# Optimization experiments

Measured on AMD Instinct MI355X. Metric: run time of the kernel, lower is better.

The kernel has to match this reference:

```python
import jax, jax.numpy as jnp
from jax import lax
import numpy as np

D_MODEL = 1024
EXP = 2
D_INNER = EXP * D_MODEL
D_STATE = 16
D_CONV = 4
DT_RANK = 64  # ceil(d_model/16), mamba default
NUM_GROUPS = 4
BSZ, SEQ = 2, 2048
EPS = 1e-5


def setup_inputs() -> dict:
    key = jax.random.key(0)
    ks = jax.random.split(key, 10)
    def n(k, shape, s=0.02):
        return jax.random.normal(k, shape, jnp.float32) * s
    return dict(
        x=jax.random.normal(ks[0], (BSZ, SEQ, D_MODEL), jnp.float32),
        ln1_g=jnp.ones((D_MODEL,), jnp.float32), ln1_b=jnp.zeros((D_MODEL,), jnp.float32),
        ln2_g=jnp.ones((D_MODEL,), jnp.float32), ln2_b=jnp.zeros((D_MODEL,), jnp.float32),
        W1=n(ks[1], (EXP * D_MODEL, D_MODEL)), b1=jnp.zeros((EXP * D_MODEL,), jnp.float32),
        W2=n(ks[2], (D_MODEL, EXP * D_MODEL)), b2=jnp.zeros((D_MODEL,), jnp.float32),
        in_proj_w=n(ks[3], (2 * D_INNER, D_MODEL)),
        conv_w=n(ks[4], (D_INNER, 1, D_CONV), 0.2), conv_b=jnp.zeros((D_INNER,), jnp.float32),
        x_proj_w=n(ks[5], (DT_RANK + 2 * D_STATE, D_INNER)),
        dt_proj_w=n(ks[6], (D_INNER, DT_RANK), 0.1), dt_proj_b=n(ks[7], (D_INNER,), 0.5),
        A_log=jnp.tile(jnp.log(jnp.arange(1, D_STATE + 1, dtype=jnp.float32)), (D_INNER, 1)),
        D_param=jnp.ones((D_INNER,), jnp.float32),
        out_proj_w=n(ks[8], (D_MODEL, D_INNER)),
    )


def _layernorm(x, g, b):
    m = jnp.mean(x, -1, keepdims=True)
    v = jnp.var(x, -1, keepdims=True)
    return (x - m) * lax.rsqrt(v + EPS) * g + b


def _ste_sign(w):
    # sign quantization with straight-through estimator (groupwise split is a no-op for sign)
    return w + lax.stop_gradient(jnp.sign(w) - w)


def _quant_act_groupwise(x, b=8):
    # groups along seq dim (x.shape[1]); gamma is the abs-max over the whole group slab
    Qb = float(2 ** (b - 1))
    B_, L, D = x.shape
    g = x.reshape(B_, NUM_GROUPS, L // NUM_GROUPS, D)
    gamma = jnp.max(jnp.abs(g), axis=(0, 2, 3), keepdims=True)
    q = jnp.clip(g * Qb / (gamma + EPS), -Qb + EPS, Qb - EPS)
    return q.reshape(B_, L, D)


def _mamba(u, in_proj_w, conv_w, conv_b, x_proj_w, dt_proj_w, dt_proj_b, A_log, D_param, out_proj_w):
    B_, L, _ = u.shape
    xz = u @ in_proj_w.T                         # [B, L, 2*d_inner]
    xs, z = jnp.split(xz, 2, axis=-1)
    # depthwise causal conv1d
    xt = jnp.transpose(xs, (0, 2, 1))            # [B, d_inner, L]
    xt = lax.conv_general_dilated(xt, conv_w, (1,), [(D_CONV - 1, 0)],
                                  feature_group_count=D_INNER,
                                  dimension_numbers=('NCH', 'OIH', 'NCH'))
    xt = xt + conv_b[None, :, None]
    xs = jax.nn.silu(jnp.transpose(xt, (0, 2, 1)))  # [B, L, d_inner]
    x_dbl = xs @ x_proj_w.T                      # [B, L, dt_rank + 2*d_state]
    dt, Bm, Cm = jnp.split(x_dbl, [DT_RANK, DT_RANK + D_STATE], axis=-1)
    dt = jax.nn.softplus(dt @ dt_proj_w.T + dt_proj_b)   # [B, L, d_inner]
    A = -jnp.exp(A_log)                          # [d_inner, d_state]

    def step(h, inp):
        dt_s, B_s, C_s, x_s = inp                # [B,di], [B,ds], [B,ds], [B,di]
        dA = jnp.exp(dt_s[..., None] * A)        # [B, di, ds]
        h = h * dA + (dt_s * x_s)[..., None] * B_s[:, None, :]
        y = jnp.einsum('bds,bs->bd', h, C_s)
        return h, y

    tm = lambda a: jnp.transpose(a, (1, 0, 2))   # time-major
    h0 = jnp.zeros((B_, D_INNER, D_STATE), u.dtype)
    _, ys = lax.scan(step, h0, (tm(dt), tm(Bm), tm(Cm), tm(xs)))
    y = jnp.transpose(ys, (1, 0, 2)) + D_param * xs
    y = y * jax.nn.silu(z)
    return y @ out_proj_w.T


def reference(x, ln1_g, ln1_b, ln2_g, ln2_b, W1, b1, W2, b2,
              in_proj_w, conv_w, conv_b, x_proj_w, dt_proj_w, dt_proj_b,
              A_log, D_param, out_proj_w):
    qW1 = _ste_sign(W1)
    qW2 = _ste_sign(W2)
    gated = jnp.clip(_layernorm(x, ln1_g, ln1_b) @ qW1.T + b1, -1.0, 1.0)  # Hardtanh
    x = x + gated @ qW2.T + b2
    qx = _quant_act_groupwise(x)
    out = qx + _mamba(_layernorm(qx, ln2_g, ln2_b), in_proj_w, conv_w, conv_b,
                      x_proj_w, dt_proj_w, dt_proj_b, A_log, D_param, out_proj_w)
    return out
```

## Files before the change

### kernel.cpp

```cpp
#include <hip/hip_runtime.h>
#include <math.h>

#define D_MODEL 1024
#define D_INNER 2048
#define D_STATE 16
#define DT_RANK 64
#define BSZ 2
#define SEQ 2048
#define NTOK (BSZ*SEQ)
#define NCH  (BSZ*D_INNER)
#define NCHUNK 64
#define CLEN 32
#define EPS 1e-5f

typedef __attribute__((ext_vector_type(8))) short short8v;
typedef __attribute__((ext_vector_type(4))) float f32x4;

__device__ __forceinline__ float sgnf(float w) {
    return (w > 0.f) ? 1.f : ((w < 0.f) ? -1.f : 0.f);
}
__device__ __forceinline__ unsigned short f2bf(float f) {
    unsigned int x = __float_as_uint(f);
    x += 0x7fffu + ((x >> 16) & 1u);
    return (unsigned short)(x >> 16);
}
__device__ __forceinline__ float bf2f(unsigned short u) {
    return __uint_as_float(((unsigned int)u) << 16);
}
__device__ __forceinline__ void stage16(const unsigned short* g, unsigned short* l) {
    __builtin_amdgcn_global_load_lds(
        (const __attribute__((address_space(1))) unsigned int*)g,
        (__attribute__((address_space(3))) unsigned int*)l, 16, 0, 0);
}
#define LDv(p) (*reinterpret_cast<const short8v*>(p))

#define F4_C1   524288
#define F4_C2   1048576
#define F4_C3   2097152
#define F4_C4   2146304
#define F4_C5   2179072
#define F4_C6   2703360
__global__ __launch_bounds__(256) void f2bf_all_kernel(
    const float* __restrict__ W1, const float* __restrict__ W2,
    const float* __restrict__ inpj, const float* __restrict__ xpj,
    const float* __restrict__ dtpj, const float* __restrict__ outpj,
    unsigned short* __restrict__ o_w1, unsigned short* __restrict__ o_w2,
    unsigned short* __restrict__ o_in, unsigned short* __restrict__ o_xp,
    unsigned short* __restrict__ o_dt, unsigned short* __restrict__ o_out,
    unsigned int* __restrict__ gma)
{
    int i = blockIdx.x * 256 + threadIdx.x;
    if (blockIdx.x == 0 && threadIdx.x < 4) gma[threadIdx.x] = 0u;
    if (i >= F4_C6) return;
    const float* src; unsigned short* dst; int off; bool sign = false;
    if (i < F4_C1)      { src = W1;   dst = o_w1;  off = i;          sign = true; }
    else if (i < F4_C2) { src = W2;   dst = o_w2;  off = i - F4_C1;  sign = true; }
    else if (i < F4_C3) { src = inpj; dst = o_in;  off = i - F4_C2; }
    else if (i < F4_C4) { src = xpj;  dst = o_xp;  off = i - F4_C3; }
    else if (i < F4_C5) { src = dtpj; dst = o_dt;  off = i - F4_C4; }
    else                { src = outpj;dst = o_out; off = i - F4_C5; }
    float4 v = reinterpret_cast<const float4*>(src)[off];
    if (sign) { v.x = sgnf(v.x); v.y = sgnf(v.y); v.z = sgnf(v.z); v.w = sgnf(v.w); }
    ushort4 o;
    o.x = f2bf(v.x); o.y = f2bf(v.y); o.z = f2bf(v.z); o.w = f2bf(v.w);
    reinterpret_cast<ushort4*>(dst)[off] = o;
}

__global__ __launch_bounds__(256) void ln_hilo_kernel(const float* __restrict__ x,
                                                      const float* __restrict__ g,
                                                      const float* __restrict__ b,
                                                      unsigned short* __restrict__ hi,
                                                      unsigned short* __restrict__ lo) {
    int row = blockIdx.x, tid = threadIdx.x;
    float4 v = reinterpret_cast<const float4*>(x + (size_t)row * D_MODEL)[tid];
    float s = v.x + v.y + v.z + v.w;
    float q = v.x*v.x + v.y*v.y + v.z*v.z + v.w*v.w;
    #pragma unroll
    for (int off = 32; off > 0; off >>= 1) { s += __shfl_down(s, off); q += __shfl_down(q, off); }
    __shared__ float rs[4], rq[4], smean, srstd;
    if ((tid & 63) == 0) { rs[tid >> 6] = s; rq[tid >> 6] = q; }
    __syncthreads();
    if (tid == 0) {
        float ts = rs[0]+rs[1]+rs[2]+rs[3], tq = rq[0]+rq[1]+rq[2]+rq[3];
        float mean = ts * (1.0f / D_MODEL);
        smean = mean;
        srstd = rsqrtf(tq * (1.0f / D_MODEL) - mean*mean + EPS);
    }
    __syncthreads();
    float mean = smean, rstd = srstd;
    float4 gg = reinterpret_cast<const float4*>(g)[tid];
    float4 bb = reinterpret_cast<const float4*>(b)[tid];
    float o[4];
    o[0] = (v.x-mean)*rstd*gg.x + bb.x; o[1] = (v.y-mean)*rstd*gg.y + bb.y;
    o[2] = (v.z-mean)*rstd*gg.z + bb.z; o[3] = (v.w-mean)*rstd*gg.w + bb.w;
    ushort4 h4, l4;
    h4.x = f2bf(o[0]); l4.x = f2bf(o[0] - bf2f(h4.x));
    h4.y = f2bf(o[1]); l4.y = f2bf(o[1] - bf2f(h4.y));
    h4.z = f2bf(o[2]); l4.z = f2bf(o[2] - bf2f(h4.z));
    h4.w = f2bf(o[3]); l4.w = f2bf(o[3] - bf2f(h4.w));
    reinterpret_cast<ushort4*>(hi + (size_t)row * D_MODEL)[tid] = h4;
    reinterpret_cast<ushort4*>(lo + (size_t)row * D_MODEL)[tid] = l4;
}

__global__ __launch_bounds__(512) void mfma_gemm256_bf16out(
    const unsigned short* __restrict__ A, const unsigned short* __restrict__ B,
    unsigned short* __restrict__ Cb, int M, int N, int K, int sA, int sC)
{
    __shared__ __align__(16) unsigned short As[2][256*64];
    __shared__ __align__(16) unsigned short Bs[2][256*64];
    const int tid = threadIdx.x, lane = tid & 63, w = tid >> 6;
    const int wm = w >> 2, wn = w & 3;
    int bx = blockIdx.x, by = blockIdx.y;
    {
        const int gx = gridDim.x, nwg = gx * gridDim.y;
        int lin = by * gx + bx;
        int nl = (lin & 7) * (nwg >> 3) + (lin >> 3);
        bx = nl % gx; by = nl / gx;
    }
    const int row0 = by * 256, col0 = bx * 256;
    const int lr = lane >> 3, lc = lane & 7;
    const int lcs = (lc ^ lr) << 3;
    const int ga = wn;
    const int h2 = wn >> 1, g2 = wm * 2 + (wn & 1);
    const int T = K >> 6;

    f32x4 acc[8][4];
    #pragma unroll
    for (int m = 0; m < 8; ++m)
        #pragma unroll
        for (int n = 0; n < 4; ++n) acc[m][n] = (f32x4){0.f,0.f,0.f,0.f};

    auto STAGE = [&](int t) {
        const int kk = t << 6, p = t & 1;
        #pragma unroll
        for (int i = 0; i < 4; ++i) {
            const int rl = wm*128 + ga*32 + i*8;
            stage16(A + (size_t)(row0 + rl + lr) * sA + kk + lcs, &As[p][rl*64]);
        }
        #pragma unroll
        for (int i = 0; i < 4; ++i) {
            const int rl = h2*128 + g2*32 + i*8;
            stage16(B + (size_t)(col0 + rl + lr) * K + kk + lcs, &Bs[p][rl*64]);
        }
    };

    STAGE(0); STAGE(1);

    const int fr = lane & 15;
    const int sw = fr & 7;
    const int q0 = (((lane >> 4)    ) ^ sw) << 3;
    const int q1 = (((lane >> 4) + 4) ^ sw) << 3;

    for (int t = 0; t < T; ++t) {
        const int p = t & 1;
        if (t + 1 < T) asm volatile("s_waitcnt vmcnt(8)" ::: "memory");
        else           asm volatile("s_waitcnt vmcnt(0)" ::: "memory");
        __builtin_amdgcn_sched_barrier(0);
        __builtin_amdgcn_s_barrier();

        const unsigned short* Ab = &As[p][(wm*128 + fr) * 64];
        const unsigned short* Bb = &Bs[p][(wn*64  + fr) * 64];
        short8v aX[4][2], bX[2][2], bY[2][2];

        #pragma unroll
        for (int m = 0; m < 4; ++m) {
            aX[m][0] = LDv(Ab + m*16*64 + q0);
            aX[m][1] = LDv(Ab + m*16*64 + q1);
        }
        #pragma unroll
        for (int n = 0; n < 2; ++n) {
            bX[n][0] = LDv(Bb + n*16*64 + q0);
            bX[n][1] = LDv(Bb + n*16*64 + q1);
        }
        __builtin_amdgcn_s_barrier();
        __builtin_amdgcn_s_setprio(1);
        #pragma unroll
        for (int m = 0; m < 4; ++m)
            #pragma unroll
            for (int n = 0; n < 2; ++n) {
                acc[m][n] = __builtin_amdgcn_mfma_f32_16x16x32_bf16(aX[m][0], bX[n][0], acc[m][n],0,0,0);
                acc[m][n] = __builtin_amdgcn_mfma_f32_16x16x32_bf16(aX[m][1], bX[n][1], acc[m][n],0,0,0);
            }
        __builtin_amdgcn_s_setprio(0);
        __builtin_amdgcn_s_barrier();
        #pragma unroll
        for (int n = 0; n < 2; ++n) {
            bY[n][0] = LDv(Bb + (n+2)*16*64 + q0);
            bY[n][1] = LDv(Bb + (n+2)*16*64 + q1);
        }
        __builtin_amdgcn_s_barrier();
        __builtin_amdgcn_s_setprio(1);
        #pragma unroll
        for (int m = 0; m < 4; ++m)
            #pragma unroll
            for (int n = 0; n < 2; ++n) {
                acc[m][n+2] = __builtin_amdgcn_mfma_f32_16x16x32_bf16(aX[m][0], bY[n][0], acc[m][n+2],0,0,0);
                acc[m][n+2] = __builtin_amdgcn_mfma_f32_16x16x32_bf16(aX[m][1], bY[n][1], acc[m][n+2],0,0,0);
            }
        __builtin_amdgcn_s_setprio(0);
        __builtin_amdgcn_s_barrier();
        #pragma unroll
        for (int m = 0; m < 4; ++m) {
            aX[m][0] = LDv(Ab + (m+4)*16*64 + q0);
            aX[m][1] = LDv(Ab + (m+4)*16*64 + q1);
        }
        __builtin_amdgcn_s_barrier();
        __builtin_amdgcn_s_setprio(1);
        #pragma unroll
        for (int m = 0; m < 4; ++m)
            #pragma unroll
            for (int n = 0; n < 2; ++n) {
                acc[m+4][n] = __builtin_amdgcn_mfma_f32_16x16x32_bf16(aX[m][0], bX[n][0], acc[m+4][n],0,0,0);
                acc[m+4][n] = __builtin_amdgcn_mfma_f32_16x16x32_bf16(aX[m][1], bX[n][1], acc[m+4][n],0,0,0);
            }
        __builtin_amdgcn_s_setprio(0);
        __builtin_amdgcn_s_barrier();
        if (t + 2 < T) STAGE(t + 2);
        __builtin_amdgcn_s_barrier();
        __builtin_amdgcn_s_setprio(1);
        #pragma unroll
        for (int m = 0; m < 4; ++m)
            #pragma unroll
            for (int n = 0; n < 2; ++n) {
                acc[m+4][n+2] = __builtin_amdgcn_mfma_f32_16x16x32_bf16(aX[m][0], bY[n][0], acc[m+4][n+2],0,0,0);
                acc[m+4][n+2] = __builtin_amdgcn_mfma_f32_16x16x32_bf16(aX[m][1], bY[n][1], acc[m+4][n+2],0,0,0);
            }
        __builtin_amdgcn_s_setprio(0);
        __builtin_amdgcn_s_barrier();
    }

    const int fc = lane & 15, r4 = (lane >> 4) * 4;
    #pragma unroll
    for (int m = 0; m < 8; ++m) {
        const int r = row0 + wm*128 + m*16 + r4;
        #pragma unroll
        for (int n = 0; n < 4; ++n) {
            const int gc = col0 + wn*64 + n*16 + fc;
            #pragma unroll
            for (int j = 0; j < 4; ++j)
                Cb[(size_t)(r + j)*sC + gc] = f2bf(acc[m][n][j]);
        }
    }
}

template<int EP, bool DUALA, int BN, bool KSPLIT>
__global__ __launch_bounds__(256) void mfma_gemm(
    const unsigned short* __restrict__ A, const unsigned short* __restrict__ A2,
    const unsigned short* __restrict__ B, float* __restrict__ C,
    unsigned short* __restrict__ Cb,
    int M, int N, int K, int sA, int sC,
    const float* __restrict__ bias, const float* __restrict__ addx, int sAdd,
    unsigned int* __restrict__ gma, int ksl)
{
    constexpr int NF = BN / 32;
    __shared__ __align__(16) unsigned short As[128*32];
    __shared__ __align__(16) unsigned short As2[DUALA ? 128*32 : 8];
    __shared__ __align__(16) unsigned short Bs[BN*32];
    __shared__ float redmax[4];
    const int tid = threadIdx.x;
    const int lane = tid & 63;
    const int w = tid >> 6;
    const int wm = w >> 1, wn = w & 1;

    int bx = blockIdx.x, by = blockIdx.y;
    if (!KSPLIT) {
        const int gx = gridDim.x;
        const int nwg = gx * gridDim.y;
        int lin = by * gx + bx;
        int nl = (lin & 7) * (nwg >> 3) + (lin >> 3);
        bx = nl % gx; by = nl / gx;
    }
    const int row0 = by * 128, col0 = bx * BN;
    const int srow = lane >> 2;
    const int scol = (lane & 3) * 8;

    int k_begin = 0, k_end = K;
    if (KSPLIT) {
        int z = blockIdx.z;
        k_begin = z * ksl; k_end = k_begin + ksl;
        C += (size_t)z * M * sC;
    }

    f32x4 acc[4][NF];
    #pragma unroll
    for (int m = 0; m < 4; ++m)
        #pragma unroll
        for (int n = 0; n < NF; ++n)
            acc[m][n] = (f32x4){0.f, 0.f, 0.f, 0.f};

    for (int k0 = k_begin; k0 < k_end; k0 += 32) {
        #pragma unroll
        for (int i = 0; i < 2; ++i) {
            const int rbase = w * 32 + i * 16;
            stage16(A + (size_t)(row0 + rbase + srow) * sA + k0 + scol, &As[rbase * 32]);
            if (DUALA)
                stage16(A2 + (size_t)(row0 + rbase + srow) * sA + k0 + scol, &As2[rbase * 32]);
        }
        #pragma unroll
        for (int i = 0; i < BN/64; ++i) {
            const int rbase = (BN == 128) ? (w * 32 + i * 16) : (w * 16);
            if (col0 + rbase < N)
                stage16(B + (size_t)(col0 + rbase + srow) * K + k0 + scol, &Bs[rbase * 32]);
        }
        __syncthreads();

        short8v af[4], bfr[NF], af2[4];
        const int fr = lane & 15, kg = (lane >> 4) * 8;
        #pragma unroll
        for (int m = 0; m < 4; ++m)
            af[m] = *reinterpret_cast<const short8v*>(&As[(wm*64 + m*16 + fr) * 32 + kg]);
        if (DUALA) {
            #pragma unroll
            for (int m = 0; m < 4; ++m)
                af2[m] = *reinterpret_cast<const short8v*>(&As2[(wm*64 + m*16 + fr) * 32 + kg]);
        }
        #pragma unroll
        for (int n = 0; n < NF; ++n)
            bfr[n] = *reinterpret_cast<const short8v*>(&Bs[(wn*(BN/2) + n*16 + fr) * 32 + kg]);

        #pragma unroll
        for (int m = 0; m < 4; ++m)
            #pragma unroll
            for (int n = 0; n < NF; ++n) {
                acc[m][n] = __builtin_amdgcn_mfma_f32_16x16x32_bf16(af[m], bfr[n], acc[m][n], 0, 0, 0);
                if (DUALA)
                    acc[m][n] = __builtin_amdgcn_mfma_f32_16x16x32_bf16(af2[m], bfr[n], acc[m][n], 0, 0, 0);
            }
        __syncthreads();
    }

    const int fc = lane & 15, r4 = (lane >> 4) * 4;
    float lmax = 0.0f;
    #pragma unroll
    for (int m = 0; m < 4; ++m) {
        const int grb = row0 + wm*64 + m*16 + r4;
        #pragma unroll
        for (int n = 0; n < NF; ++n) {
            const int gc = col0 + wn*(BN/2) + n*16 + fc;
            if (gc >= N) continue;
            #pragma unroll
            for (int j = 0; j < 4; ++j) {
                const int r = grb + j;
                float v = acc[m][n][j];
                if (EP == 0) {
                    C[(size_t)r*sC + gc] = v;
                } else if (EP == 1) {
                    v += bias[gc];
                    v = fminf(1.0f, fmaxf(-1.0f, v));
                    Cb[(size_t)r*sC + gc] = f2bf(v);
                } else if (EP == 3) {
                    float t = v + bias[gc];
                    t = fmaxf(t, 0.0f) + log1pf(__expf(-fabsf(t)));
                    Cb[(size_t)r*sC + gc] = f2bf(t);
                } else if (EP == 4) {
                    C[(size_t)r*sC + gc] = v + addx[(size_t)r*sAdd + gc];
                } else if (EP == 6) {
                    Cb[(size_t)r*sC + gc] = f2bf(v);
                } else {
                    v += bias[gc] + addx[(size_t)r*sAdd + gc];
                    C[(size_t)r*sC + gc] = v;
                    lmax = fmaxf(lmax, fabsf(v));
                }
            }
        }
    }
    if (EP == 7) {
        #pragma unroll
        for (int off = 32; off > 0; off >>= 1) lmax = fmaxf(lmax, __shfl_down(lmax, off));
        if (lane == 0) redmax[w] = lmax;
        __syncthreads();
        if (tid == 0) {
            float t = fmaxf(fmaxf(redmax[0], redmax[1]), fmaxf(redmax[2], redmax[3]));
            int g = (row0 & (SEQ - 1)) >> 9;
            atomicMax(gma + g, __float_as_uint(t));
        }
    }
}

__global__ __launch_bounds__(256) void xproj_combine_kernel(
    const float* __restrict__ part,
    float* __restrict__ xdbl,
    unsigned short* __restrict__ xdt)
{
    int i = blockIdx.x * 256 + threadIdx.x;
    if (i >= NTOK * 24) return;
    const size_t stride = (size_t)NTOK * 96 / 4;
    float4 v0 = reinterpret_cast<const float4*>(part)[i];
    float4 v1 = reinterpret_cast<const float4*>(part)[i + stride];
    float4 v2 = reinterpret_cast<const float4*>(part)[i + 2*stride];
    float4 v3 = reinterpret_cast<const float4*>(part)[i + 3*stride];
    float4 o;
    o.x = (v0.x + v1.x) + (v2.x + v3.x);
    o.y = (v0.y + v1.y) + (v2.y + v3.y);
    o.z = (v0.z + v1.z) + (v2.z + v3.z);
    o.w = (v0.w + v1.w) + (v2.w + v3.w);
    reinterpret_cast<float4*>(xdbl)[i] = o;
    int row = i / 24, c4 = i % 24;
    if (c4 < 16) {
        ushort4 u;
        u.x = f2bf(o.x); u.y = f2bf(o.y); u.z = f2bf(o.z); u.w = f2bf(o.w);
        reinterpret_cast<ushort4*>(xdt + (size_t)row * 64)[c4] = u;
    }
}

__global__ __launch_bounds__(256) void quant_ln_kernel(
    const float* __restrict__ x2, const unsigned int* __restrict__ gamma_bits,
    const float* __restrict__ g, const float* __restrict__ b,
    float* __restrict__ qx, unsigned short* __restrict__ u)
{
    int row = blockIdx.x, tid = threadIdx.x;
    int grp = (row & (SEQ - 1)) >> 9;
    float gamma = __uint_as_float(gamma_bits[grp]);
    float scale = 128.0f / (gamma + EPS);
    const float lo = -128.0f + EPS, hi = 128.0f - EPS;
    float4 v = reinterpret_cast<const float4*>(x2 + (size_t)row * D_MODEL)[tid];
    float4 qv;
    qv.x = fminf(hi, fmaxf(lo, v.x * scale));
    qv.y = fminf(hi, fmaxf(lo, v.y * scale));
    qv.z = fminf(hi, fmaxf(lo, v.z * scale));
    qv.w = fminf(hi, fmaxf(lo, v.w * scale));
    reinterpret_cast<float4*>(qx + (size_t)row * D_MODEL)[tid] = qv;
    float s = qv.x + qv.y + qv.z + qv.w;
    float q = qv.x*qv.x + qv.y*qv.y + qv.z*qv.z + qv.w*qv.w;
    #pragma unroll
    for (int off = 32; off > 0; off >>= 1) { s += __shfl_down(s, off); q += __shfl_down(q, off); }
    __shared__ float rs[4], rq[4], smean, srstd;
    if ((tid & 63) == 0) { rs[tid >> 6] = s; rq[tid >> 6] = q; }
    __syncthreads();
    if (tid == 0) {
        float ts = rs[0]+rs[1]+rs[2]+rs[3], tq = rq[0]+rq[1]+rq[2]+rq[3];
        float mean = ts * (1.0f / D_MODEL);
        smean = mean;
        srstd = rsqrtf(tq * (1.0f / D_MODEL) - mean*mean + EPS);
    }
    __syncthreads();
    float mean = smean, rstd = srstd;
    float4 gg = reinterpret_cast<const float4*>(g)[tid];
    float4 bb = reinterpret_cast<const float4*>(b)[tid];
    ushort4 o;
    o.x = f2bf((qv.x-mean)*rstd*gg.x + bb.x);
    o.y = f2bf((qv.y-mean)*rstd*gg.y + bb.y);
    o.z = f2bf((qv.z-mean)*rstd*gg.z + bb.z);
    o.w = f2bf((qv.w-mean)*rstd*gg.w + bb.w);
    reinterpret_cast<ushort4*>(u + (size_t)row * D_MODEL)[tid] = o;
}

__global__ __launch_bounds__(256) void conv_silu_kernel(const unsigned short* __restrict__ xz,
                                                        const float* __restrict__ conv_w,
                                                        const float* __restrict__ conv_b,
                                                        unsigned short* __restrict__ xcb) {
    int c = blockIdx.x * 256 + threadIdx.x;
    int m = blockIdx.y;
    int b = m >> 11, l = m & (SEQ - 1);
    float4 w4 = reinterpret_cast<const float4*>(conv_w)[c];
    float wv[4] = {w4.x, w4.y, w4.z, w4.w};
    float s = conv_b[c];
    const unsigned short* base = xz + ((size_t)b * SEQ) * 4096 + c;
    #pragma unroll
    for (int k = 0; k < 4; ++k) {
        int ll = l - 3 + k;
        if (ll >= 0) s += bf2f(base[(size_t)ll * 4096]) * wv[k];
    }
    float sig = 1.0f / (1.0f + __expf(-s));
    xcb[(size_t)m * D_INNER + c] = f2bf(s * sig);
}

__device__ __forceinline__ void make_dA(float dA[D_STATE], float dtv,
                                        const float* a, bool pw) {
    if (pw) {
        dA[0] = __expf(dtv * a[0]);
        #pragma unroll
        for (int s = 1; s < D_STATE; ++s) dA[s] = dA[s>>1] * dA[(s-1)>>1];
    } else {
        #pragma unroll
        for (int s = 0; s < D_STATE; ++s) dA[s] = __expf(dtv * a[s]);
    }
}

__global__ __launch_bounds__(256) void scan_partial_kernel(
    const unsigned short* __restrict__ dt, const unsigned short* __restrict__ xcb,
    const float* __restrict__ xdbl, const float* __restrict__ A_log,
    float* __restrict__ Lbuf, float* __restrict__ Sbuf)
{
    int gtid = blockIdx.x * 256 + threadIdx.x;
    int ch = gtid & (NCH - 1);
    int c  = gtid >> 12;
    int b = ch >> 11, d = ch & (D_INNER - 1);
    float a[D_STATE], h[D_STATE];
    bool pw = true;
    #pragma unroll
    for (int s = 0; s < D_STATE; ++s) {
        a[s] = -__expf(A_log[(size_t)d * D_STATE + s]);
        h[s] = 0.0f;
    }
    #pragma unroll
    for (int s = 1; s < D_STATE; ++s)
        pw = pw && (fabsf(a[s] - a[0]*(float)(s+1)) <= 1e-3f * fabsf(a[s]));

    size_t m0 = (size_t)b * SEQ + (size_t)c * CLEN;
    float Ssum = 0.0f;

    float dt_n = bf2f(dt[m0 * D_INNER + d]);
    float x_n  = bf2f(xcb[m0 * D_INNER + d]);
    float4 B_n[4];
    {
        const float* xd = xdbl + m0 * 96;
        #pragma unroll
        for (int i = 0; i < 4; ++i)
            B_n[i] = *reinterpret_cast<const float4*>(xd + DT_RANK + 4*i);
    }

    for (int l = 0; l < CLEN; ++l) {
        float dtv = dt_n, xv = x_n;
        float Bc[D_STATE];
        #pragma unroll
        for (int i = 0; i < 4; ++i) {
            Bc[4*i+0] = B_n[i].x; Bc[4*i+1] = B_n[i].y; Bc[4*i+2] = B_n[i].z; Bc[4*i+3] = B_n[i].w;
        }
        if (l + 1 < CLEN) {
            size_t m1 = m0 + l + 1;
            dt_n = bf2f(dt[m1 * D_INNER + d]);
            x_n  = bf2f(xcb[m1 * D_INNER + d]);
            const float* xd = xdbl + m1 * 96;
            #pragma unroll
            for (int i = 0; i < 4; ++i)
                B_n[i] = *reinterpret_cast<const float4*>(xd + DT_RANK + 4*i);
        }
        Ssum += dtv;
        float dx = dtv * xv;
        float dA[D_STATE];
        make_dA(dA, dtv, a, pw);
        #pragma unroll
        for (int s = 0; s < D_STATE; ++s)
            h[s] = h[s] * dA[s] + dx * Bc[s];
    }
    float4* Lp = reinterpret_cast<float4*>(Lbuf + (size_t)c * (NCH * D_STATE) + (size_t)ch * D_STATE);
    Lp[0] = make_float4(h[0], h[1], h[2], h[3]);
    Lp[1] = make_float4(h[4], h[5], h[6], h[7]);
    Lp[2] = make_float4(h[8], h[9], h[10], h[11]);
    Lp[3] = make_float4(h[12], h[13], h[14], h[15]);
    Sbuf[(size_t)c * NCH + ch] = Ssum;
}

__global__ __launch_bounds__(256) void scan_combine_kernel(
    float* __restrict__ LH, const float* __restrict__ Sbuf,
    const float* __restrict__ A_log)
{
    int gtid = blockIdx.x * 256 + threadIdx.x;
    int s = gtid & (D_STATE - 1);
    int ch = gtid >> 4;
    int d = ch & (D_INNER - 1);
    float a = -__expf(A_log[(size_t)d * D_STATE + s]);
    float h = 0.0f;
    #pragma unroll 4
    for (int c = 0; c < NCHUNK; ++c) {
        size_t idx = (size_t)c * (NCH * D_STATE) + (size_t)ch * D_STATE + s;
        float loc = LH[idx];
        LH[idx] = h;
        float P = __expf(a * Sbuf[(size_t)c * NCH + ch]);
        h = h * P + loc;
    }
}

__global__ __launch_bounds__(256) void scan_final_kernel(
    const unsigned short* __restrict__ dt, const unsigned short* __restrict__ xcb,
    const unsigned short* __restrict__ xzb, const float* __restrict__ xdbl,
    const float* __restrict__ A_log, const float* __restrict__ D_param,
    const float* __restrict__ Hin, unsigned short* __restrict__ yb)
{
    int gtid = blockIdx.x * 256 + threadIdx.x;
    int ch = gtid & (NCH - 1);
    int c  = gtid >> 12;
    int b = ch >> 11, d = ch & (D_INNER - 1);
    float a[D_STATE], h[D_STATE];
    {
        const float4* Hp = reinterpret_cast<const float4*>(
            Hin + (size_t)c * (NCH * D_STATE) + (size_t)ch * D_STATE);
        float4 h0 = Hp[0], h1 = Hp[1], h2 = Hp[2], h3 = Hp[3];
        h[0]=h0.x; h[1]=h0.y; h[2]=h0.z; h[3]=h0.w;
        h[4]=h1.x; h[5]=h1.y; h[6]=h1.z; h[7]=h1.w;
        h[8]=h2.x; h[9]=h2.y; h[10]=h2.z; h[11]=h2.w;
        h[12]=h3.x; h[13]=h3.y; h[14]=h3.z; h[15]=h3.w;
    }
    bool pw = true;
    #pragma unroll
    for (int s = 0; s < D_STATE; ++s)
        a[s] = -__expf(A_log[(size_t)d * D_STATE + s]);
    #pragma unroll
    for (int s = 1; s < D_STATE; ++s)
        pw = pw && (fabsf(a[s] - a[0]*(float)(s+1)) <= 1e-3f * fabsf(a[s]));
    float Dp = D_param[d];

    size_t m0 = (size_t)b * SEQ + (size_t)c * CLEN;
    float dt_n = bf2f(dt[m0 * D_INNER + d]);
    float x_n  = bf2f(xcb[m0 * D_INNER + d]);
    float z_n  = bf2f(xzb[m0 * 4096 + D_INNER + d]);
    float4 B_n[4], C_n[4];
    {
        const float* xd = xdbl + m0 * 96;
        #pragma unroll
        for (int i = 0; i < 4; ++i) {
            B_n[i] = *reinterpret_cast<const float4*>(xd + DT_RANK + 4*i);
            C_n[i] = *reinterpret_cast<const float4*>(xd + DT_RANK + D_STATE + 4*i);
        }
    }

    for (int l = 0; l < CLEN; ++l) {
        float dtv = dt_n, xv = x_n, zv = z_n;
        float Bc[D_STATE], Cc[D_STATE];
        #pragma unroll
        for (int i = 0; i < 4; ++i) {
            Bc[4*i+0] = B_n[i].x; Bc[4*i+1] = B_n[i].y; Bc[4*i+2] = B_n[i].z; Bc[4*i+3] = B_n[i].w;
            Cc[4*i+0] = C_n[i].x; Cc[4*i+1] = C_n[i].y; Cc[4*i+2] = C_n[i].z; Cc[4*i+3] = C_n[i].w;
        }
        if (l + 1 < CLEN) {
            size_t m1 = m0 + l + 1;
            dt_n = bf2f(dt[m1 * D_INNER + d]);
            x_n  = bf2f(xcb[m1 * D_INNER + d]);
            z_n  = bf2f(xzb[m1 * 4096 + D_INNER + d]);
            const float* xd = xdbl + m1 * 96;
            #pragma unroll
            for (int i = 0; i < 4; ++i) {
                B_n[i] = *reinterpret_cast<const float4*>(xd + DT_RANK + 4*i);
                C_n[i] = *reinterpret_cast<const float4*>(xd + DT_RANK + D_STATE + 4*i);
            }
        }
        float dx = dtv * xv;
        float yv = 0.0f;
        float dA[D_STATE];
        make_dA(dA, dtv, a, pw);
        #pragma unroll
        for (int s = 0; s < D_STATE; ++s) {
            h[s] = h[s] * dA[s] + dx * Bc[s];
            yv += h[s] * Cc[s];
        }
        yv += Dp * xv;
        float sig = 1.0f / (1.0f + __expf(-zv));
        yb[(m0 + l) * D_INNER + d] = f2bf(yv * (zv * sig));
    }
}

extern "C" void kernel_launch(void* const* d_in, const int* in_sizes, int n_in,
                              void* d_out, int out_size, void* d_ws, size_t ws_size,
                              hipStream_t stream) {
    const float* x         = (const float*)d_in[0];
    const float* ln1_g     = (const float*)d_in[1];
    const float* ln1_b     = (const float*)d_in[2];
    const float* ln2_g     = (const float*)d_in[3];
    const float* ln2_b     = (const float*)d_in[4];
    const float* W1        = (const float*)d_in[5];
    const float* b1        = (const float*)d_in[6];
    const float* W2        = (const float*)d_in[7];
    const float* b2        = (const float*)d_in[8];
    const float* in_proj   = (const float*)d_in[9];
    const float* conv_w    = (const float*)d_in[10];
    const float* conv_b    = (const float*)d_in[11];
    const float* x_proj    = (const float*)d_in[12];
    const float* dt_proj   = (const float*)d_in[13];
    const float* dt_proj_b = (const float*)d_in[14];
    const float* A_log     = (const float*)d_in[15];
    const float* D_param   = (const float*)d_in[16];
    const float* out_proj  = (const float*)d_in[17];
    float* out = (float*)d_out;

    char* ws = (char*)d_ws;
    float*          f_x2   = (float*)         (ws + 0);
    unsigned short* b_xz   = (unsigned short*)(ws + 16777216);
    unsigned short* b_dt   = (unsigned short*)(ws + 50331648);
    float*          f_xdbl = (float*)         (ws + 83886080);
    float*          f_L    = (float*)         (ws + 85458944);
    float*          f_xp   = f_L;
    float*          f_S    = (float*)         (ws + 102236160);
    unsigned int*   f_gamma= (unsigned int*)  (ws + 103284736);
    unsigned short* b_a1hi = (unsigned short*)(ws + 103284800);
    unsigned short* b_a1lo = b_a1hi + 4194304;
    unsigned short* b_y    = b_a1hi;
    unsigned short* b_gated= (unsigned short*)(ws + 120062016);
    unsigned short* b_xc   = b_gated;
    unsigned short* b_u    = (unsigned short*)(ws + 136839232);
    unsigned short* b_xdt  = b_u;
    unsigned short* b_w1s  = (unsigned short*)(ws + 145227840);
    unsigned short* b_w2s  = (unsigned short*)(ws + 149422144);
    unsigned short* b_inpj = (unsigned short*)(ws + 153616448);
    unsigned short* b_xpj  = (unsigned short*)(ws + 162005056);
    unsigned short* b_dtpj = (unsigned short*)(ws + 162398272);
    unsigned short* b_outpj= (unsigned short*)(ws + 162660416);

    dim3 b256(256);

    f2bf_all_kernel<<<dim3((F4_C6 + 255)/256), b256, 0, stream>>>(
        W1, W2, in_proj, x_proj, dt_proj, out_proj,
        b_w1s, b_w2s, b_inpj, b_xpj, b_dtpj, b_outpj, f_gamma);

    ln_hilo_kernel<<<dim3(NTOK), b256, 0, stream>>>(x, ln1_g, ln1_b, b_a1hi, b_a1lo);
    mfma_gemm<1, true, 128, false><<<dim3(16, 32), b256, 0, stream>>>(
        b_a1hi, b_a1lo, b_w1s, nullptr, b_gated, NTOK, D_INNER, D_MODEL, D_MODEL, D_INNER,
        b1, nullptr, 0, nullptr, 0);
    mfma_gemm<7, false, 128, false><<<dim3(8, 32), b256, 0, stream>>>(
        b_gated, nullptr, b_w2s, f_x2, nullptr, NTOK, D_MODEL, D_INNER, D_INNER, D_MODEL,
        b2, x, D_MODEL, f_gamma, 0);
    quant_ln_kernel<<<dim3(NTOK), b256, 0, stream>>>(f_x2, f_gamma, ln2_g, ln2_b, f_x2, b_u);
    mfma_gemm256_bf16out<<<dim3(16, 16), dim3(512), 0, stream>>>(
        b_u, b_inpj, b_xz, NTOK, 2*D_INNER, D_MODEL, D_MODEL, 2*D_INNER);
    conv_silu_kernel<<<dim3(D_INNER/256, NTOK), b256, 0, stream>>>(b_xz, conv_w, conv_b, b_xc);
    mfma_gemm<0, false, 128, true><<<dim3(1, 32, 4), b256, 0, stream>>>(
        b_xc, nullptr, b_xpj, f_xp, nullptr, NTOK, DT_RANK + 2*D_STATE, D_INNER, D_INNER,
        DT_RANK + 2*D_STATE, nullptr, nullptr, 0, nullptr, 512);
    xproj_combine_kernel<<<dim3((NTOK*24 + 255)/256), b256, 0, stream>>>(f_xp, f_xdbl, b_xdt);
    mfma_gemm<3, false, 64, false><<<dim3(32, 32), b256, 0, stream>>>(
        b_xdt, nullptr, b_dtpj, nullptr, b_dt, NTOK, D_INNER, DT_RANK, DT_RANK, D_INNER,
        dt_proj_b, nullptr, 0, nullptr, 0);
    scan_partial_kernel<<<dim3(NCH*NCHUNK/256), b256, 0, stream>>>(
        b_dt, b_xc, f_xdbl, A_log, f_L, f_S);
    scan_combine_kernel<<<dim3(NCH*D_STATE/256), b256, 0, stream>>>(f_L, f_S, A_log);
    scan_final_kernel<<<dim3(NCH*NCHUNK/256), b256, 0, stream>>>(
        b_dt, b_xc, b_xz, f_xdbl, A_log, D_param, f_L, b_y);
    mfma_gemm<4, false, 128, false><<<dim3(8, 32), b256, 0, stream>>>(
        b_y, nullptr, b_outpj, out, nullptr, NTOK, D_MODEL, D_INNER, D_INNER, D_MODEL,
        nullptr, f_x2, D_MODEL, nullptr, 0);
}
```

Baseline: 474.1 us.

## Split-K the two D_MODEL-output GEMMs with separate combine kernels

The W2 GEMM and the out_proj GEMM (4096x1024 output, K=2048) previously ran on only 256 workgroups. Both now use a 4-way split-K, launching 1024 workgroups that write fp32 partials into the workspace. A new combine kernel sums the partials and adds the bias and residual; for W2 it also computes the per-group absmax with an atomicMax. This trades under-filled CUs for about 64MB of extra partial-buffer traffic and two additional kernel launches.

```diff
diff --git a/kernel.cpp b/kernel.cpp
--- a/kernel.cpp
+++ b/kernel.cpp
@@ -249,14 +249,12 @@
     const unsigned short* __restrict__ B, float* __restrict__ C,
     unsigned short* __restrict__ Cb,
     int M, int N, int K, int sA, int sC,
-    const float* __restrict__ bias, const float* __restrict__ addx, int sAdd,
-    unsigned int* __restrict__ gma, int ksl)
+    const float* __restrict__ bias, int ksl)
 {
     constexpr int NF = BN / 32;
     __shared__ __align__(16) unsigned short As[128*32];
     __shared__ __align__(16) unsigned short As2[DUALA ? 128*32 : 8];
     __shared__ __align__(16) unsigned short Bs[BN*32];
-    __shared__ float redmax[4];
     const int tid = threadIdx.x;
     const int lane = tid & 63;
     const int w = tid >> 6;
@@ -330,7 +328,6 @@
     }
 
     const int fc = lane & 15, r4 = (lane >> 4) * 4;
-    float lmax = 0.0f;
     #pragma unroll
     for (int m = 0; m < 4; ++m) {
         const int grb = row0 + wm*64 + m*16 + r4;
@@ -352,27 +349,46 @@
                     float t = v + bias[gc];
                     t = fmaxf(t, 0.0f) + log1pf(__expf(-fabsf(t)));
                     Cb[(size_t)r*sC + gc] = f2bf(t);
-                } else if (EP == 4) {
-                    C[(size_t)r*sC + gc] = v + addx[(size_t)r*sAdd + gc];
-                } else if (EP == 6) {
-                    Cb[(size_t)r*sC + gc] = f2bf(v);
-                } else {
-                    v += bias[gc] + addx[(size_t)r*sAdd + gc];
-                    C[(size_t)r*sC + gc] = v;
-                    lmax = fmaxf(lmax, fabsf(v));
                 }
             }
         }
     }
-    if (EP == 7) {
-        #pragma unroll
-        for (int off = 32; off > 0; off >>= 1) lmax = fmaxf(lmax, __shfl_down(lmax, off));
-        if (lane == 0) redmax[w] = lmax;
+}
+
+template<bool ABSMAX>
+__global__ __launch_bounds__(256) void splitk_combine_kernel(
+    const float* __restrict__ part, const float* __restrict__ bias,
+    const float* __restrict__ addx, float* __restrict__ C,
+    unsigned int* __restrict__ gma)
+{
+    const int row = blockIdx.x, tid = threadIdx.x;
+    const size_t stride = (size_t)NTOK * D_MODEL / 4;
+    const size_t i = (size_t)row * 256 + tid;
+    float4 v0 = reinterpret_cast<const float4*>(part)[i];
+    float4 v1 = reinterpret_cast<const float4*>(part)[i + stride];
+    float4 v2 = reinterpret_cast<const float4*>(part)[i + 2*stride];
+    float4 v3 = reinterpret_cast<const float4*>(part)[i + 3*stride];
+    float4 ax = reinterpret_cast<const float4*>(addx)[i];
+    float4 o;
+    o.x = (v0.x + v1.x) + (v2.x + v3.x) + ax.x;
+    o.y = (v0.y + v1.y) + (v2.y + v3.y) + ax.y;
+    o.z = (v0.z + v1.z) + (v2.z + v3.z) + ax.z;
+    o.w = (v0.w + v1.w) + (v2.w + v3.w) + ax.w;
+    if (bias) {
+        float4 b4 = reinterpret_cast<const float4*>(bias)[tid];
+        o.x += b4.x; o.y += b4.y; o.z += b4.z; o.w += b4.w;
+    }
+    reinterpret_cast<float4*>(C)[i] = o;
+    if (ABSMAX) {
+        float m = fmaxf(fmaxf(fabsf(o.x), fabsf(o.y)), fmaxf(fabsf(o.z), fabsf(o.w)));
+        #pragma unroll
+        for (int off = 32; off > 0; off >>= 1) m = fmaxf(m, __shfl_down(m, off));
+        __shared__ float red[4];
+        if ((tid & 63) == 0) red[tid >> 6] = m;
         __syncthreads();
         if (tid == 0) {
-            float t = fmaxf(fmaxf(redmax[0], redmax[1]), fmaxf(redmax[2], redmax[3]));
-            int g = (row0 & (SEQ - 1)) >> 9;
-            atomicMax(gma + g, __float_as_uint(t));
+            float t = fmaxf(fmaxf(red[0], red[1]), fmaxf(red[2], red[3]));
+            atomicMax(gma + ((row & (SEQ - 1)) >> 9), __float_as_uint(t));
         }
     }
 }
@@ -667,6 +683,7 @@
     float*          f_x2   = (float*)         (ws + 0);
     unsigned short* b_xz   = (unsigned short*)(ws + 16777216);
     unsigned short* b_dt   = (unsigned short*)(ws + 50331648);
+    float*          f_p4   = (float*)         (ws + 16777216);
     float*          f_xdbl = (float*)         (ws + 83886080);
     float*          f_L    = (float*)         (ws + 85458944);
     float*          f_xp   = f_L;
@@ -695,27 +712,29 @@
     ln_hilo_kernel<<<dim3(NTOK), b256, 0, stream>>>(x, ln1_g, ln1_b, b_a1hi, b_a1lo);
     mfma_gemm<1, true, 128, false><<<dim3(16, 32), b256, 0, stream>>>(
         b_a1hi, b_a1lo, b_w1s, nullptr, b_gated, NTOK, D_INNER, D_MODEL, D_MODEL, D_INNER,
-        b1, nullptr, 0, nullptr, 0);
-    mfma_gemm<7, false, 128, false><<<dim3(8, 32), b256, 0, stream>>>(
-        b_gated, nullptr, b_w2s, f_x2, nullptr, NTOK, D_MODEL, D_INNER, D_INNER, D_MODEL,
-        b2, x, D_MODEL, f_gamma, 0);
+        b1, 0);
+    mfma_gemm<0, false, 128, true><<<dim3(8, 32, 4), b256, 0, stream>>>(
+        b_gated, nullptr, b_w2s, f_p4, nullptr, NTOK, D_MODEL, D_INNER, D_INNER, D_MODEL,
+        nullptr, 512);
+    splitk_combine_kernel<true><<<dim3(NTOK), b256, 0, stream>>>(f_p4, b2, x, f_x2, f_gamma);
     quant_ln_kernel<<<dim3(NTOK), b256, 0, stream>>>(f_x2, f_gamma, ln2_g, ln2_b, f_x2, b_u);
     mfma_gemm256_bf16out<<<dim3(16, 16), dim3(512), 0, stream>>>(
         b_u, b_inpj, b_xz, NTOK, 2*D_INNER, D_MODEL, D_MODEL, 2*D_INNER);
     conv_silu_kernel<<<dim3(D_INNER/256, NTOK), b256, 0, stream>>>(b_xz, conv_w, conv_b, b_xc);
     mfma_gemm<0, false, 128, true><<<dim3(1, 32, 4), b256, 0, stream>>>(
         b_xc, nullptr, b_xpj, f_xp, nullptr, NTOK, DT_RANK + 2*D_STATE, D_INNER, D_INNER,
-        DT_RANK + 2*D_STATE, nullptr, nullptr, 0, nullptr, 512);
+        DT_RANK + 2*D_STATE, nullptr, 512);
     xproj_combine_kernel<<<dim3((NTOK*24 + 255)/256), b256, 0, stream>>>(f_xp, f_xdbl, b_xdt);
     mfma_gemm<3, false, 64, false><<<dim3(32, 32), b256, 0, stream>>>(
         b_xdt, nullptr, b_dtpj, nullptr, b_dt, NTOK, D_INNER, DT_RANK, DT_RANK, D_INNER,
-        dt_proj_b, nullptr, 0, nullptr, 0);
+        dt_proj_b, 0);
     scan_partial_kernel<<<dim3(NCH*NCHUNK/256), b256, 0, stream>>>(
         b_dt, b_xc, f_xdbl, A_log, f_L, f_S);
     scan_combine_kernel<<<dim3(NCH*D_STATE/256), b256, 0, stream>>>(f_L, f_S, A_log);
     scan_final_kernel<<<dim3(NCH*NCHUNK/256), b256, 0, stream>>>(
         b_dt, b_xc, b_xz, f_xdbl, A_log, D_param, f_L, b_y);
-    mfma_gemm<4, false, 128, false><<<dim3(8, 32), b256, 0, stream>>>(
-        b_y, nullptr, b_outpj, out, nullptr, NTOK, D_MODEL, D_INNER, D_INNER, D_MODEL,
-        nullptr, f_x2, D_MODEL, nullptr, 0);
-}
+    mfma_gemm<0, false, 128, true><<<dim3(8, 32, 4), b256, 0, stream>>>(
+        b_y, nullptr, b_outpj, f_p4, nullptr, NTOK, D_MODEL, D_INNER, D_INNER, D_MODEL,
+        nullptr, 512);
+    splitk_combine_kernel<false><<<dim3(NTOK), b256, 0, stream>>>(f_p4, nullptr, f_x2, out, nullptr);
+}
```

Result: slower. 519.5 us (+9.6%).

## Add 512-thread double-buffered ping-pong GEMM for W2 and out_proj projections

Applied to the files above, without the earlier changes.

Introduces a new 128x128-tile GEMM kernel with 8 waves, 64-wide K steps, double-buffered LDS with XOR swizzling, and interleaved load/MFMA phases using setprio and barriers. It replaces the older 256-thread single-buffered GEMM for the K=2048 W2 and out_proj GEMMs, aiming to overlap global loads with MFMA work and raise occupancy. The old kernel's unused epilogues are removed. More LDS per block and more barrier phases could reduce occupancy or add sync overhead.

```diff
diff --git a/kernel.cpp b/kernel.cpp
--- a/kernel.cpp
+++ b/kernel.cpp
@@ -243,20 +243,164 @@
     }
 }
 
+template<int EP>
+__global__ __launch_bounds__(512) void mfma_gemm128_8ph(
+    const unsigned short* __restrict__ A, const unsigned short* __restrict__ B,
+    float* __restrict__ C, int M, int N, int K, int sA, int sC,
+    const float* __restrict__ bias, const float* __restrict__ addx, int sAdd,
+    unsigned int* __restrict__ gma)
+{
+    __shared__ __align__(16) unsigned short As[2][128*64];
+    __shared__ __align__(16) unsigned short Bs[2][128*64];
+    __shared__ float redmax[8];
+    const int tid = threadIdx.x, lane = tid & 63, w = tid >> 6;
+    const int wm = w >> 2, wn = w & 3;
+    int bx = blockIdx.x, by = blockIdx.y;
+    {
+        const int gx = gridDim.x, nwg = gx * gridDim.y;
+        int lin = by * gx + bx;
+        int nl = (lin & 7) * (nwg >> 3) + (lin >> 3);
+        bx = nl % gx; by = nl / gx;
+    }
+    const int row0 = by * 128, col0 = bx * 128;
+    const int lr = lane >> 3, lc = lane & 7;
+    const int lcs = (lc ^ lr) << 3;
+    const int T = K >> 6;
+
+    f32x4 acc[4][2];
+    #pragma unroll
+    for (int m = 0; m < 4; ++m) {
+        acc[m][0] = (f32x4){0.f,0.f,0.f,0.f};
+        acc[m][1] = (f32x4){0.f,0.f,0.f,0.f};
+    }
+
+    auto STAGE = [&](int t) {
+        const int kk = t << 6, p = t & 1;
+        #pragma unroll
+        for (int i = 0; i < 2; ++i) {
+            const int rl = w*16 + i*8;
+            stage16(A + (size_t)(row0 + rl + lr) * sA + kk + lcs, &As[p][rl*64]);
+        }
+        #pragma unroll
+        for (int i = 0; i < 2; ++i) {
+            const int rl = w*16 + i*8;
+            stage16(B + (size_t)(col0 + rl + lr) * K + kk + lcs, &Bs[p][rl*64]);
+        }
+    };
+
+    STAGE(0); STAGE(1);
+
+    const int fr = lane & 15;
+    const int sw = fr & 7;
+    const int q0 = (((lane >> 4)    ) ^ sw) << 3;
+    const int q1 = (((lane >> 4) + 4) ^ sw) << 3;
+
+    for (int t = 0; t < T; ++t) {
+        const int p = t & 1;
+        if (t + 1 < T) asm volatile("s_waitcnt vmcnt(4)" ::: "memory");
+        else           asm volatile("s_waitcnt vmcnt(0)" ::: "memory");
+        __builtin_amdgcn_sched_barrier(0);
+        __builtin_amdgcn_s_barrier();
+
+        const unsigned short* Ab = &As[p][(wm*64 + fr) * 64];
+        const unsigned short* Bb = &Bs[p][(wn*32 + fr) * 64];
+        short8v aX[4][2], bX[2][2];
+
+        #pragma unroll
+        for (int m = 0; m < 2; ++m) {
+            aX[m][0] = LDv(Ab + m*16*64 + q0);
+            aX[m][1] = LDv(Ab + m*16*64 + q1);
+        }
+        #pragma unroll
+        for (int n = 0; n < 2; ++n) {
+            bX[n][0] = LDv(Bb + n*16*64 + q0);
+            bX[n][1] = LDv(Bb + n*16*64 + q1);
+        }
+        __builtin_amdgcn_s_barrier();
+        __builtin_amdgcn_s_setprio(1);
+        #pragma unroll
+        for (int m = 0; m < 2; ++m)
+            #pragma unroll
+            for (int n = 0; n < 2; ++n) {
+                acc[m][n] = __builtin_amdgcn_mfma_f32_16x16x32_bf16(aX[m][0], bX[n][0], acc[m][n],0,0,0);
+                acc[m][n] = __builtin_amdgcn_mfma_f32_16x16x32_bf16(aX[m][1], bX[n][1], acc[m][n],0,0,0);
+            }
+        __builtin_amdgcn_s_setprio(0);
+        __builtin_amdgcn_s_barrier();
+        #pragma unroll
+        for (int m = 0; m < 2; ++m) {
+            aX[m+2][0] = LDv(Ab + (m+2)*16*64 + q0);
+            aX[m+2][1] = LDv(Ab + (m+2)*16*64 + q1);
+        }
+        __builtin_amdgcn_s_barrier();
+        __builtin_amdgcn_s_setprio(1);
+        #pragma unroll
+        for (int m = 0; m < 2; ++m) {
+            acc[m+2][0] = __builtin_amdgcn_mfma_f32_16x16x32_bf16(aX[m+2][0], bX[0][0], acc[m+2][0],0,0,0);
+            acc[m+2][0] = __builtin_amdgcn_mfma_f32_16x16x32_bf16(aX[m+2][1], bX[0][1], acc[m+2][0],0,0,0);
+        }
+        __builtin_amdgcn_s_setprio(0);
+        __builtin_amdgcn_s_barrier();
+        if (t + 2 < T) STAGE(t + 2);
+        __builtin_amdgcn_s_barrier();
+        __builtin_amdgcn_s_setprio(1);
+        #pragma unroll
+        for (int m = 0; m < 2; ++m) {
+            acc[m+2][1] = __builtin_amdgcn_mfma_f32_16x16x32_bf16(aX[m+2][0], bX[1][0], acc[m+2][1],0,0,0);
+            acc[m+2][1] = __builtin_amdgcn_mfma_f32_16x16x32_bf16(aX[m+2][1], bX[1][1], acc[m+2][1],0,0,0);
+        }
+        __builtin_amdgcn_s_setprio(0);
+        __builtin_amdgcn_s_barrier();
+    }
+
+    const int fc = lane & 15, r4 = (lane >> 4) * 4;
+    float lmax = 0.0f;
+    #pragma unroll
+    for (int m = 0; m < 4; ++m) {
+        const int rb = row0 + wm*64 + m*16 + r4;
+        #pragma unroll
+        for (int n = 0; n < 2; ++n) {
+            const int gc = col0 + wn*32 + n*16 + fc;
+            #pragma unroll
+            for (int j = 0; j < 4; ++j) {
+                const int r = rb + j;
+                float v = acc[m][n][j];
+                if (EP == 7) {
+                    v += bias[gc] + addx[(size_t)r*sAdd + gc];
+                    C[(size_t)r*sC + gc] = v;
+                    lmax = fmaxf(lmax, fabsf(v));
+                } else {
+                    C[(size_t)r*sC + gc] = v + addx[(size_t)r*sAdd + gc];
+                }
+            }
+        }
+    }
+    if (EP == 7) {
+        #pragma unroll
+        for (int off = 32; off > 0; off >>= 1) lmax = fmaxf(lmax, __shfl_down(lmax, off));
+        if (lane == 0) redmax[w] = lmax;
+        __syncthreads();
+        if (tid == 0) {
+            float t = redmax[0];
+            #pragma unroll
+            for (int i = 1; i < 8; ++i) t = fmaxf(t, redmax[i]);
+            atomicMax(gma + ((row0 & (SEQ - 1)) >> 9), __float_as_uint(t));
+        }
+    }
+}
+
 template<int EP, bool DUALA, int BN, bool KSPLIT>
 __global__ __launch_bounds__(256) void mfma_gemm(
     const unsigned short* __restrict__ A, const unsigned short* __restrict__ A2,
     const unsigned short* __restrict__ B, float* __restrict__ C,
     unsigned short* __restrict__ Cb,
     int M, int N, int K, int sA, int sC,
-    const float* __restrict__ bias, const float* __restrict__ addx, int sAdd,
-    unsigned int* __restrict__ gma, int ksl)
+    const float* __restrict__ bias, int ksl)
 {
     constexpr int NF = BN / 32;
     __shared__ __align__(16) unsigned short As[128*32];
     __shared__ __align__(16) unsigned short As2[DUALA ? 128*32 : 8];
     __shared__ __align__(16) unsigned short Bs[BN*32];
-    __shared__ float redmax[4];
     const int tid = threadIdx.x;
     const int lane = tid & 63;
     const int w = tid >> 6;
@@ -330,7 +474,6 @@
     }
 
     const int fc = lane & 15, r4 = (lane >> 4) * 4;
-    float lmax = 0.0f;
     #pragma unroll
     for (int m = 0; m < 4; ++m) {
         const int grb = row0 + wm*64 + m*16 + r4;
@@ -352,27 +495,8 @@
                     float t = v + bias[gc];
                     t = fmaxf(t, 0.0f) + log1pf(__expf(-fabsf(t)));
                     Cb[(size_t)r*sC + gc] = f2bf(t);
-                } else if (EP == 4) {
-                    C[(size_t)r*sC + gc] = v + addx[(size_t)r*sAdd + gc];
-                } else if (EP == 6) {
-                    Cb[(size_t)r*sC + gc] = f2bf(v);
-                } else {
-                    v += bias[gc] + addx[(size_t)r*sAdd + gc];
-                    C[(size_t)r*sC + gc] = v;
-                    lmax = fmaxf(lmax, fabsf(v));
                 }
             }
-        }
-    }
-    if (EP == 7) {
-        #pragma unroll
-        for (int off = 32; off > 0; off >>= 1) lmax = fmaxf(lmax, __shfl_down(lmax, off));
-        if (lane == 0) redmax[w] = lmax;
-        __syncthreads();
-        if (tid == 0) {
-            float t = fmaxf(fmaxf(redmax[0], redmax[1]), fmaxf(redmax[2], redmax[3]));
-            int g = (row0 & (SEQ - 1)) >> 9;
-            atomicMax(gma + g, __float_as_uint(t));
         }
     }
 }
@@ -695,27 +819,27 @@
     ln_hilo_kernel<<<dim3(NTOK), b256, 0, stream>>>(x, ln1_g, ln1_b, b_a1hi, b_a1lo);
     mfma_gemm<1, true, 128, false><<<dim3(16, 32), b256, 0, stream>>>(
         b_a1hi, b_a1lo, b_w1s, nullptr, b_gated, NTOK, D_INNER, D_MODEL, D_MODEL, D_INNER,
-        b1, nullptr, 0, nullptr, 0);
-    mfma_gemm<7, false, 128, false><<<dim3(8, 32), b256, 0, stream>>>(
-        b_gated, nullptr, b_w2s, f_x2, nullptr, NTOK, D_MODEL, D_INNER, D_INNER, D_MODEL,
-        b2, x, D_MODEL, f_gamma, 0);
+        b1, 0);
+    mfma_gemm128_8ph<7><<<dim3(8, 32), dim3(512), 0, stream>>>(
+        b_gated, b_w2s, f_x2, NTOK, D_MODEL, D_INNER, D_INNER, D_MODEL,
+        b2, x, D_MODEL, f_gamma);
     quant_ln_kernel<<<dim3(NTOK), b256, 0, stream>>>(f_x2, f_gamma, ln2_g, ln2_b, f_x2, b_u);
     mfma_gemm256_bf16out<<<dim3(16, 16), dim3(512), 0, stream>>>(
         b_u, b_inpj, b_xz, NTOK, 2*D_INNER, D_MODEL, D_MODEL, 2*D_INNER);
     conv_silu_kernel<<<dim3(D_INNER/256, NTOK), b256, 0, stream>>>(b_xz, conv_w, conv_b, b_xc);
     mfma_gemm<0, false, 128, true><<<dim3(1, 32, 4), b256, 0, stream>>>(
         b_xc, nullptr, b_xpj, f_xp, nullptr, NTOK, DT_RANK + 2*D_STATE, D_INNER, D_INNER,
-        DT_RANK + 2*D_STATE, nullptr, nullptr, 0, nullptr, 512);
+        DT_RANK + 2*D_STATE, nullptr, 512);
     xproj_combine_kernel<<<dim3((NTOK*24 + 255)/256), b256, 0, stream>>>(f_xp, f_xdbl, b_xdt);
     mfma_gemm<3, false, 64, false><<<dim3(32, 32), b256, 0, stream>>>(
         b_xdt, nullptr, b_dtpj, nullptr, b_dt, NTOK, D_INNER, DT_RANK, DT_RANK, D_INNER,
-        dt_proj_b, nullptr, 0, nullptr, 0);
+        dt_proj_b, 0);
     scan_partial_kernel<<<dim3(NCH*NCHUNK/256), b256, 0, stream>>>(
         b_dt, b_xc, f_xdbl, A_log, f_L, f_S);
     scan_combine_kernel<<<dim3(NCH*D_STATE/256), b256, 0, stream>>>(f_L, f_S, A_log);
     scan_final_kernel<<<dim3(NCH*NCHUNK/256), b256, 0, stream>>>(
         b_dt, b_xc, b_xz, f_xdbl, A_log, D_param, f_L, b_y);
-    mfma_gemm<4, false, 128, false><<<dim3(8, 32), b256, 0, stream>>>(
-        b_y, nullptr, b_outpj, out, nullptr, NTOK, D_MODEL, D_INNER, D_INNER, D_MODEL,
-        nullptr, f_x2, D_MODEL, nullptr, 0);
-}
+    mfma_gemm128_8ph<4><<<dim3(8, 32), dim3(512), 0, stream>>>(
+        b_y, b_outpj, out, NTOK, D_MODEL, D_INNER, D_INNER, D_MODEL,
+        nullptr, f_x2, D_MODEL, nullptr);
+}
```

Result: faster. 456.3 us (-3.8%).
